# Optimization experiments

Hardware: AMD Instinct MI355X
Metric: run time of the kernel (lower is better)

Reference implementation:

```python
import jax, jax.numpy as jnp
from jax import lax
import numpy as np

N_QUBITS = 4
N_LAYERS = 2


def _apply_gate(state, M, w):
    # state: [B, 2,2,2,2]; M: [2,2] shared or [B,2,2] batched; acts on wire w
    s = jnp.moveaxis(state, w + 1, 1)
    if M.ndim == 3:
        s = jnp.einsum('bij,bj...->bi...', M, s)
    else:
        s = jnp.einsum('ij,bj...->bi...', M, s)
    return jnp.moveaxis(s, 1, w + 1)


def _apply_cnot(state, c, t):
    # c < t always (chain CNOTs). Move control axis to 1; target axis (t+1) unchanged.
    s = jnp.moveaxis(state, c + 1, 1)
    s0 = s[:, 0]
    s1 = jnp.flip(s[:, 1], axis=t)  # target axis after dropping axis1 is t+1-1 = t
    s = jnp.stack([s0, s1], axis=1)
    return jnp.moveaxis(s, 1, c + 1)


def _quantum_head(q_input, qparams):
    # q_input: [B, n_qubits] rotation angles; qparams: [n_layers, n_qubits, 3]
    B = q_input.shape[0]
    state = jnp.zeros((B, 2 ** N_QUBITS), jnp.complex64).at[:, 0].set(1.0)
    state = state.reshape((B,) + (2,) * N_QUBITS)
    # RY feature map (batched matrices)
    for i in range(N_QUBITS):
        th = q_input[:, i]
        c, s = jnp.cos(th / 2), jnp.sin(th / 2)
        M = jnp.stack([jnp.stack([c, -s], -1), jnp.stack([s, c], -1)], -2)  # [B,2,2]
        state = _apply_gate(state, M.astype(jnp.complex64), i)
    # variational layers
    for layer in range(N_LAYERS):
        for i in range(N_QUBITS):
            phi = qparams[layer, i, 0]
            th = qparams[layer, i, 1]
            om = qparams[layer, i, 2]
            c, s = jnp.cos(th / 2), jnp.sin(th / 2)
            hs, hd = 0.5 * (phi + om), 0.5 * (phi - om)
            M = jnp.stack([
                jnp.stack([jnp.exp(-1j * hs) * c, -jnp.exp(1j * hd) * s]),
                jnp.stack([jnp.exp(-1j * hd) * s, jnp.exp(1j * hs) * c]),
            ])  # [2,2] shared across batch (Rot = RZ(om) RY(th) RZ(phi))
            state = _apply_gate(state, M.astype(jnp.complex64), i)
        for i in range(N_QUBITS - 1):
            state = _apply_cnot(state, i, i + 1)
    # <Z_0> = P(q0=0) - P(q0=1)
    probs = state.real ** 2 + state.imag ** 2
    probs = probs.reshape(B, 2, -1)
    return probs[:, 0].sum(-1) - probs[:, 1].sum(-1)


def _maxpool21(x):
    return lax.reduce_window(x, -np.inf, lax.max, (1, 1, 2, 2), (1, 1, 1, 1), 'VALID')


def setup_inputs() -> dict:
    key = jax.random.key(0)
    ks = jax.random.split(key, 8)
    r = lambda k, s, sc: jax.random.normal(k, s, jnp.float32) * sc
    return {
        'inputs': jax.random.normal(ks[0], (128, 3, 250, 250), jnp.float32),
        'conv1_w': r(ks[1], (6, 3, 5, 5), 0.1),
        'conv1_b': jnp.zeros((6,), jnp.float32),
        'conv2_w': r(ks[2], (15, 6, 3, 3), 0.1),
        'conv2_b': jnp.zeros((15,), jnp.float32),
        'fc1_w': r(ks[3], (120, 55815), 0.004),
        'fc1_b': jnp.zeros((120,), jnp.float32),
        'fc2_w': r(ks[4], (84, 120), 0.09),
        'fc2_b': jnp.zeros((84,), jnp.float32),
        'fc3_w': r(ks[5], (1, 84), 0.1),
        'fc3_b': jnp.zeros((1,), jnp.float32),
        'qparams': jax.random.normal(ks[6], (N_LAYERS, N_QUBITS, 3), jnp.float32),
    }


def reference(inputs, conv1_w, conv1_b, conv2_w, conv2_b, fc1_w, fc1_b,
              fc2_w, fc2_b, fc3_w, fc3_b, qparams):
    dn = ('NCHW', 'OIHW', 'NCHW')
    x = lax.conv_general_dilated(inputs, conv1_w, (2, 2), [(1, 1), (1, 1)],
                                 dimension_numbers=dn) + conv1_b[None, :, None, None]
    x = _maxpool21(jax.nn.relu(x))          # [B,6,123,123]
    x = lax.conv_general_dilated(x, conv2_w, (2, 2), [(1, 1), (1, 1)],
                                 dimension_numbers=dn) + conv2_b[None, :, None, None]
    x = _maxpool21(jax.nn.relu(x))          # [B,15,61,61]
    x = x.reshape(x.shape[0], -1)           # [B,55815]
    x = jax.nn.relu(x @ fc1_w.T + fc1_b)
    x = jax.nn.relu(x @ fc2_w.T + fc2_b)
    x = (x @ fc3_w.T + fc3_b)[:, 0]         # [B]
    q_input = jnp.repeat(x[:, None], N_QUBITS, axis=1)
    q_out = _quantum_head(q_input, qparams)  # [B]
    probs = 0.5 * (q_out + 1.0)
    return jnp.stack([probs, 1.0 - probs], axis=-1)
```

## Files before the change

kernel.cpp:

```cpp
#include <hip/hip_runtime.h>

#define SPLITK 256
#define FC1_K 55815
#define KP 55816

__device__ __forceinline__ unsigned short f2bf(float f) {
    unsigned u = __float_as_uint(f);
    return (unsigned short)((u + 0x7FFFu + ((u >> 16) & 1u)) >> 16);
}

__global__ __launch_bounds__(256) void conv1f_k(const float* __restrict__ in,
                                                const float* __restrict__ w,
                                                const float* __restrict__ bias,
                                                float* __restrict__ out) {
    __shared__ float sbuf[4608];
    const int tc = blockIdx.x, tr = blockIdx.y, b = blockIdx.z;
    const int pr0 = tr * 31, pc0 = tc * 31;
    const int tid = threadIdx.x;
    const int i = tid >> 4, j = tid & 15;
    const float* inb = in + (size_t)b * 187500;
    const int ir0 = 2 * pr0 - 1, ic0 = 2 * pc0 - 1;

    float acc[6][2][2];
    #pragma unroll
    for (int o = 0; o < 6; ++o) {
        float bv = bias[o];
        acc[o][0][0] = bv; acc[o][0][1] = bv; acc[o][1][0] = bv; acc[o][1][1] = bv;
    }

    float stg[18];
    auto load_ch = [&](int c) {
        const float* cp = inb + c * 62500;
        int y = tid / 68;
        int x = tid - y * 68;
        #pragma unroll
        for (int it = 0; it < 18; ++it) {
            int gr = ir0 + y, gc = ic0 + x;
            float v = 0.0f;
            if ((unsigned)gr < 250u && (unsigned)gc < 250u)
                v = cp[gr * 250 + gc];
            stg[it] = v;
            x += 52; y += 3;
            if (x >= 68) { x -= 68; ++y; }
        }
    };
    auto write_ch = [&]() {
        #pragma unroll
        for (int it = 0; it < 18; ++it) sbuf[tid + it * 256] = stg[it];
    };
    auto compute_ch = [&](int c) {
        #pragma unroll
        for (int wr = 0; wr < 7; ++wr) {
            const float* rp = &sbuf[(4 * i + wr) * 68 + 4 * j];
            float row[7];
            float4 v4 = *(const float4*)rp;
            float2 v2 = *(const float2*)(rp + 4);
            row[0] = v4.x; row[1] = v4.y; row[2] = v4.z; row[3] = v4.w;
            row[4] = v2.x; row[5] = v2.y; row[6] = rp[6];
            #pragma unroll
            for (int o = 0; o < 6; ++o) {
                #pragma unroll
                for (int kw = 0; kw < 5; ++kw) {
                    if (wr <= 4) {
                        float wv = w[o * 75 + c * 25 + wr * 5 + kw];
                        acc[o][0][0] = fmaf(row[kw], wv, acc[o][0][0]);
                        acc[o][0][1] = fmaf(row[kw + 2], wv, acc[o][0][1]);
                    }
                    if (wr >= 2) {
                        float wv = w[o * 75 + c * 25 + (wr - 2) * 5 + kw];
                        acc[o][1][0] = fmaf(row[kw], wv, acc[o][1][0]);
                        acc[o][1][1] = fmaf(row[kw + 2], wv, acc[o][1][1]);
                    }
                }
            }
        }
    };

    load_ch(0); write_ch();
    __syncthreads();
    load_ch(1); compute_ch(0);
    __syncthreads();
    write_ch();
    __syncthreads();
    load_ch(2); compute_ch(1);
    __syncthreads();
    write_ch();
    __syncthreads();
    compute_ch(2);
    __syncthreads();

    const int gr0 = pr0 + 2 * i, gc0 = pc0 + 2 * j;
    const bool r1in = (2 * i + 1 < 31) && (gr0 + 1 < 123);
    const bool c1in = (2 * j + 1 < 31) && (gc0 + 1 < 123);
    const bool r0in = gr0 < 123, c0in = gc0 < 123;
    #pragma unroll
    for (int g = 0; g < 2; ++g) {
        #pragma unroll
        for (int oo = 0; oo < 3; ++oo)
            #pragma unroll
            for (int di = 0; di < 2; ++di)
                #pragma unroll
                for (int dj = 0; dj < 2; ++dj)
                    sbuf[(oo * 32 + 2 * i + di) * 33 + (2 * j + dj)] =
                        fmaxf(acc[g * 3 + oo][di][dj], 0.0f);
        __syncthreads();
        #pragma unroll
        for (int oo = 0; oo < 3; ++oo) {
            int o = g * 3 + oo;
            const float* p0 = &sbuf[(oo * 32 + 2 * i) * 33 + 2 * j];
            float c00 = p0[0],  c01 = p0[1],  c02 = p0[2];
            float c10 = p0[33], c11 = p0[34], c12 = p0[35];
            float c20 = p0[66], c21 = p0[67], c22 = p0[68];
            float* orow = out + ((size_t)(b * 6 + o) * 123 + gr0) * 123 + gc0;
            if (r0in && c0in) orow[0]   = fmaxf(fmaxf(c00, c01), fmaxf(c10, c11));
            if (r0in && c1in) orow[1]   = fmaxf(fmaxf(c01, c02), fmaxf(c11, c12));
            if (r1in && c0in) orow[123] = fmaxf(fmaxf(c10, c11), fmaxf(c20, c21));
            if (r1in && c1in) orow[124] = fmaxf(fmaxf(c11, c12), fmaxf(c21, c22));
        }
        __syncthreads();
    }
}

__global__ __launch_bounds__(256) void conv2f_k(const float* __restrict__ in,
                                                const float* __restrict__ w,
                                                const float* __restrict__ bias,
                                                unsigned short* __restrict__ out) {
    __shared__ float smem[2000];
    const int tc = blockIdx.x, tr = blockIdx.y, b = blockIdx.z;
    const int pr0 = tr * 15, pc0 = tc * 15;
    const int tid = threadIdx.x;
    const int wv = tid >> 6, lane = tid & 63;
    const int ti = tid >> 4, tj = tid & 15;
    const int tl = ti & 3;
    float* wreg = smem + wv * 320;
    float* halo = smem + 1280;
    const float* inb = in + (size_t)b * 6 * 15129;
    const int irw = 2 * pr0 - 1 + 8 * wv;
    const int ic0 = 2 * pc0 - 1;
    const bool safe = (tr >= 1 && tr <= 3) && (tc >= 1 && tc <= 3);

    int off[5];
    unsigned msk = 0u;
    {
        int y = (lane >= 34) ? 1 : 0;
        int x = lane - 34 * y;
        #pragma unroll
        for (int it = 0; it < 5; ++it) {
            int gr = irw + y, gc = ic0 + x;
            bool valid = ((unsigned)gr < 123u) && ((unsigned)gc < 123u);
            off[it] = valid ? (gr * 123 + gc) : 0;
            msk |= (valid ? 1u : 0u) << it;
            x += 30; ++y;
            if (x >= 34) { x -= 34; ++y; }
        }
    }

    float acc[15];
    #pragma unroll
    for (int o = 0; o < 15; ++o) acc[o] = bias[o];

    for (int c = 0; c < 6; ++c) {
        const float* cp = inb + c * 15129;
        if (safe) {
            #pragma unroll
            for (int it = 0; it < 5; ++it) wreg[lane + it * 64] = cp[off[it]];
        } else {
            #pragma unroll
            for (int it = 0; it < 5; ++it) {
                float v = 0.0f;
                if ((msk >> it) & 1u) v = cp[off[it]];
                wreg[lane + it * 64] = v;
            }
        }
        #pragma unroll
        for (int kh = 0; kh < 3; ++kh) {
            const float* r = &wreg[(2 * tl + kh) * 34 + 2 * tj];
            float a0 = r[0], a1 = r[1], a2 = r[2];
            #pragma unroll
            for (int o = 0; o < 15; ++o) {
                const float* wr_ = &w[o * 54 + c * 9 + kh * 3];
                acc[o] = fmaf(a0, wr_[0], acc[o]);
                acc[o] = fmaf(a1, wr_[1], acc[o]);
                acc[o] = fmaf(a2, wr_[2], acc[o]);
            }
        }
    }

    if (tl == 0 && wv > 0) {
        #pragma unroll
        for (int o = 0; o < 15; ++o)
            halo[(wv - 1) * 240 + o * 16 + tj] = acc[o];
    }
    __syncthreads();

    const int gr = pr0 + ti, gc = pc0 + tj;
    const bool valid = (ti < 15) && (tj < 15) && (gr < 61) && (gc < 61);
    const bool lastrow = (tl == 3);
    const int hb = (wv < 2 ? wv : 2) * 240;
    #pragma unroll
    for (int o = 0; o < 15; ++o) {
        float c00 = acc[o];
        float c01 = __shfl(acc[o], lane + 1);
        float s10 = __shfl(acc[o], lane + 16);
        float s11 = __shfl(acc[o], lane + 17);
        float h10 = halo[hb + o * 16 + tj];
        float h11 = halo[hb + o * 16 + (tj + 1 > 15 ? 15 : tj + 1)];
        float c10 = lastrow ? h10 : s10;
        float c11 = lastrow ? h11 : s11;
        float m = fmaxf(fmaxf(fmaxf(c00, c01), fmaxf(c10, c11)), 0.0f);
        if (valid) out[(size_t)b * KP + o * 3721 + gr * 61 + gc] = f2bf(m);
    }
}

__global__ __launch_bounds__(256) void wcvt_k(const float* __restrict__ W,
                                              unsigned short* __restrict__ Wb) {
    const int n = blockIdx.y;
    const float* src = W + (size_t)n * FC1_K;
    unsigned int* dst = (unsigned int*)(Wb + (size_t)n * KP);
    int base = blockIdx.x * 2048 + threadIdx.x * 2;
    #pragma unroll
    for (int p = 0; p < 4; ++p) {
        int k2 = base + p * 512;
        if (k2 < FC1_K) {
            float v0 = src[k2];
            float v1 = (k2 + 1 < FC1_K) ? src[k2 + 1] : 0.0f;
            dst[k2 >> 1] = (unsigned)f2bf(v0) | ((unsigned)f2bf(v1) << 16);
        }
    }
}

__global__ __launch_bounds__(256) void fc1_k(const unsigned short* __restrict__ Xb,
                                             const unsigned short* __restrict__ Wb,
                                             float* __restrict__ P) {
    using short8 = __attribute__((ext_vector_type(8))) short;
    using f32x4 = __attribute__((ext_vector_type(4))) float;
    __shared__ unsigned short Xs[2][128][40];
    __shared__ unsigned short Ws[2][128][40];
    const int s = blockIdx.x;
    const int ks = s * 224;
    const int ke = min(ks + 224, FC1_K);
    const int tid = threadIdx.x;
    const int row = tid >> 1, cb = (tid & 1) * 16;
    const int wv = tid >> 6, lane = tid & 63;
    const int kb = lane >> 4, lr = lane & 15;

    f32x4 acc[2][8];
    #pragma unroll
    for (int mt = 0; mt < 2; ++mt)
        #pragma unroll
        for (int nt = 0; nt < 8; ++nt)
            acc[mt][nt] = (f32x4){0.f, 0.f, 0.f, 0.f};

    const int nsteps = (ke > ks) ? ((ke - ks + 31) >> 5) : 0;

    auto stage = [&](int buf, int st) {
        const int k0 = ks + st * 32;
        const int krem = ke - k0;
        const unsigned short* xsrc = Xb + (size_t)row * KP + k0 + cb;
        #pragma unroll
        for (int q = 0; q < 2; ++q) {
            int g = cb + q * 8;
            if (g + 8 <= krem) {
                *(uint4*)&Xs[buf][row][g] = *(const uint4*)(xsrc + q * 8);
            } else {
                #pragma unroll
                for (int jj = 0; jj < 8; ++jj)
                    Xs[buf][row][g + jj] = (g + jj < krem) ? xsrc[q * 8 + jj] : (unsigned short)0;
            }
        }
        if (row < 120) {
            const unsigned short* wsrc = Wb + (size_t)row * KP + k0 + cb;
            #pragma unroll
            for (int q = 0; q < 2; ++q) {
                int g = cb + q * 8;
                if (g + 8 <= krem) {
                    *(uint4*)&Ws[buf][row][g] = *(const uint4*)(wsrc + q * 8);
                } else {
                    #pragma unroll
                    for (int jj = 0; jj < 8; ++jj)
                        Ws[buf][row][g + jj] = (g + jj < krem) ? wsrc[q * 8 + jj] : (unsigned short)0;
                }
            }
        } else {
            uint4 z = {0u, 0u, 0u, 0u};
            *(uint4*)&Ws[buf][row][cb] = z;
            *(uint4*)&Ws[buf][row][cb + 8] = z;
        }
    };

    if (nsteps > 0) stage(0, 0);
    int cur = 0;
    for (int st = 0; st < nsteps; ++st) {
        __syncthreads();
        if (st + 1 < nsteps) stage(cur ^ 1, st + 1);
        short8 afr[2];
        #pragma unroll
        for (int mt = 0; mt < 2; ++mt)
            afr[mt] = *(const short8*)&Xs[cur][(wv * 2 + mt) * 16 + lr][kb * 8];
        #pragma unroll
        for (int nt = 0; nt < 8; ++nt) {
            short8 bfr = *(const short8*)&Ws[cur][nt * 16 + lr][kb * 8];
            #pragma unroll
            for (int mt = 0; mt < 2; ++mt)
                acc[mt][nt] = __builtin_amdgcn_mfma_f32_16x16x32_bf16(afr[mt], bfr, acc[mt][nt], 0, 0, 0);
        }
        cur ^= 1;
    }

    float* Pp = P + (size_t)s * 15360;
    #pragma unroll
    for (int mt = 0; mt < 2; ++mt)
        #pragma unroll
        for (int nt = 0; nt < 8; ++nt)
            #pragma unroll
            for (int r = 0; r < 4; ++r) {
                int m = (wv * 2 + mt) * 16 + kb * 4 + r;
                int n = nt * 16 + lr;
                if (n < 120) Pp[m * 120 + n] = acc[mt][nt][r];
            }
}

__global__ __launch_bounds__(512) void tail_k(const float* __restrict__ P,
                                              const float* __restrict__ f1b,
                                              const float* __restrict__ f2w,
                                              const float* __restrict__ f2b,
                                              const float* __restrict__ f3w,
                                              const float* __restrict__ f3b,
                                              const float* __restrict__ qp,
                                              float* __restrict__ out) {
    __shared__ float red[4][120];
    __shared__ float x1[120];
    __shared__ float x2[84];
    int b = blockIdx.x, tid = threadIdx.x;
    if (tid < 480) {
        int part = tid / 120;
        int n = tid - part * 120;
        const float* p = P + (size_t)b * 120 + n;
        float acc = 0.0f;
        #pragma unroll 8
        for (int s = part; s < SPLITK; s += 4)
            acc += p[(size_t)s * 15360];
        red[part][n] = acc;
    }
    __syncthreads();
    if (tid < 120)
        x1[tid] = fmaxf((red[0][tid] + red[1][tid]) + (red[2][tid] + red[3][tid]) + f1b[tid], 0.0f);
    __syncthreads();
    if (tid < 84) {
        float acc = f2b[tid];
        const float* wr = f2w + tid * 120;
        #pragma unroll 4
        for (int n = 0; n < 120; ++n) acc = fmaf(x1[n], wr[n], acc);
        x2[tid] = fmaxf(acc, 0.0f);
    }
    __syncthreads();
    if (tid == 0) {
        float x = f3b[0];
        for (int m = 0; m < 84; ++m) x = fmaf(x2[m], f3w[m], x);
        float sr[16], si[16];
        #pragma unroll
        for (int i = 0; i < 16; ++i) { sr[i] = 0.0f; si[i] = 0.0f; }
        sr[0] = 1.0f;
        float c0 = cosf(0.5f * x), s0 = sinf(0.5f * x);
        #pragma unroll
        for (int w = 0; w < 4; ++w) {
            int mask = 8 >> w;
            #pragma unroll
            for (int idx = 0; idx < 16; ++idx) {
                if (idx & mask) continue;
                int i1 = idx | mask;
                float a0r = sr[idx], a0i = si[idx], a1r = sr[i1], a1i = si[i1];
                sr[idx] = c0 * a0r - s0 * a1r;  si[idx] = c0 * a0i - s0 * a1i;
                sr[i1]  = s0 * a0r + c0 * a1r;  si[i1]  = s0 * a0i + c0 * a1i;
            }
        }
        for (int layer = 0; layer < 2; ++layer) {
            #pragma unroll
            for (int w = 0; w < 4; ++w) {
                int gi = (layer * 4 + w) * 3;
                float phi = qp[gi], th = qp[gi + 1], om = qp[gi + 2];
                float hs = 0.5f * (phi + om), hd = 0.5f * (phi - om);
                float ct = cosf(0.5f * th), st = sinf(0.5f * th);
                float chs = cosf(hs), shs = sinf(hs);
                float chd = cosf(hd), shd = sinf(hd);
                float m00r = chs * ct,  m00i = -shs * ct;
                float m01r = -chd * st, m01i = -shd * st;
                float m10r = chd * st,  m10i = -shd * st;
                float m11r = chs * ct,  m11i = shs * ct;
                int mask = 8 >> w;
                #pragma unroll
                for (int idx = 0; idx < 16; ++idx) {
                    if (idx & mask) continue;
                    int i1 = idx | mask;
                    float a0r = sr[idx], a0i = si[idx], a1r = sr[i1], a1i = si[i1];
                    sr[idx] = m00r * a0r - m00i * a0i + m01r * a1r - m01i * a1i;
                    si[idx] = m00r * a0i + m00i * a0r + m01r * a1i + m01i * a1r;
                    sr[i1]  = m10r * a0r - m10i * a0i + m11r * a1r - m11i * a1i;
                    si[i1]  = m10r * a0i + m10i * a0r + m11r * a1i + m11i * a1r;
                }
            }
            #pragma unroll
            for (int cw = 0; cw < 3; ++cw) {
                int cm = 8 >> cw, tm = 8 >> (cw + 1);
                #pragma unroll
                for (int idx = 0; idx < 16; ++idx) {
                    if ((idx & cm) && !(idx & tm)) {
                        int i1 = idx | tm;
                        float tr = sr[idx]; sr[idx] = sr[i1]; sr[i1] = tr;
                        float ti = si[idx]; si[idx] = si[i1]; si[i1] = ti;
                    }
                }
            }
        }
        float q = 0.0f;
        #pragma unroll
        for (int idx = 0; idx < 16; ++idx) {
            float p2 = sr[idx] * sr[idx] + si[idx] * si[idx];
            q += (idx < 8) ? p2 : -p2;
        }
        float pr = 0.5f * (q + 1.0f);
        out[2 * b] = pr;
        out[2 * b + 1] = 1.0f - pr;
    }
}

extern "C" void kernel_launch(void* const* d_in, const int* in_sizes, int n_in,
                              void* d_out, int out_size, void* d_ws, size_t ws_size,
                              hipStream_t stream) {
    const float* inp = (const float*)d_in[0];
    const float* c1w = (const float*)d_in[1];
    const float* c1b = (const float*)d_in[2];
    const float* c2w = (const float*)d_in[3];
    const float* c2b = (const float*)d_in[4];
    const float* f1w = (const float*)d_in[5];
    const float* f1b = (const float*)d_in[6];
    const float* f2w = (const float*)d_in[7];
    const float* f2b = (const float*)d_in[8];
    const float* f3w = (const float*)d_in[9];
    const float* f3b = (const float*)d_in[10];
    const float* qp  = (const float*)d_in[11];
    float* out = (float*)d_out;
    float* ws = (float*)d_ws;

    float* B = ws;
    unsigned short* Db = (unsigned short*)(ws + 11619072);
    float* P = ws + 15191296;
    unsigned short* Wb = (unsigned short*)(ws + 19123456);

    wcvt_k<<<dim3(28, 120), 256, 0, stream>>>(f1w, Wb);
    conv1f_k<<<dim3(4, 4, 128), 256, 0, stream>>>(inp, c1w, c1b, B);
    conv2f_k<<<dim3(5, 5, 128), 256, 0, stream>>>(B, c2w, c2b, Db);
    fc1_k<<<dim3(SPLITK), 256, 0, stream>>>(Db, Wb, P);
    tail_k<<<128, 512, 0, stream>>>(P, f1b, f2w, f2b, f3w, f3b, qp, out);
}
```

Baseline: 144.0 us.

## Fuse fc1 weight bf16 conversion into GEMM staging; process two images per conv2 block

Drops the separate weight-conversion kernel. fc1 now reads the fp32 weights directly and packs them to bf16 while staging into shared memory, which removes one launch and the round trip of the bf16 weight copy through memory. In exchange, fc1 reads twice the weight bytes and uses scalar, bounds-checked loads instead of 16-byte vector loads. conv2 blocks now loop over two images each with half the grid, and add an extra barrier per image.

```diff
diff --git a/kernel.cpp b/kernel.cpp
--- a/kernel.cpp
+++ b/kernel.cpp
@@ -126,7 +126,7 @@
                                                 const float* __restrict__ bias,
                                                 unsigned short* __restrict__ out) {
     __shared__ float smem[2000];
-    const int tc = blockIdx.x, tr = blockIdx.y, b = blockIdx.z;
+    const int tc = blockIdx.x, tr = blockIdx.y, b0 = blockIdx.z;
     const int pr0 = tr * 15, pc0 = tc * 15;
     const int tid = threadIdx.x;
     const int wv = tid >> 6, lane = tid & 63;
@@ -134,7 +134,6 @@
     const int tl = ti & 3;
     float* wreg = smem + wv * 320;
     float* halo = smem + 1280;
-    const float* inb = in + (size_t)b * 6 * 15129;
     const int irw = 2 * pr0 - 1 + 8 * wv;
     const int ic0 = 2 * pc0 - 1;
     const bool safe = (tr >= 1 && tr <= 3) && (tc >= 1 && tc <= 3);
@@ -155,82 +154,71 @@
         }
     }
 
-    float acc[15];
-    #pragma unroll
-    for (int o = 0; o < 15; ++o) acc[o] = bias[o];
-
-    for (int c = 0; c < 6; ++c) {
-        const float* cp = inb + c * 15129;
-        if (safe) {
-            #pragma unroll
-            for (int it = 0; it < 5; ++it) wreg[lane + it * 64] = cp[off[it]];
-        } else {
-            #pragma unroll
-            for (int it = 0; it < 5; ++it) {
-                float v = 0.0f;
-                if ((msk >> it) & 1u) v = cp[off[it]];
-                wreg[lane + it * 64] = v;
-            }
-        }
-        #pragma unroll
-        for (int kh = 0; kh < 3; ++kh) {
-            const float* r = &wreg[(2 * tl + kh) * 34 + 2 * tj];
-            float a0 = r[0], a1 = r[1], a2 = r[2];
-            #pragma unroll
-            for (int o = 0; o < 15; ++o) {
-                const float* wr_ = &w[o * 54 + c * 9 + kh * 3];
-                acc[o] = fmaf(a0, wr_[0], acc[o]);
-                acc[o] = fmaf(a1, wr_[1], acc[o]);
-                acc[o] = fmaf(a2, wr_[2], acc[o]);
-            }
-        }
-    }
-
-    if (tl == 0 && wv > 0) {
-        #pragma unroll
-        for (int o = 0; o < 15; ++o)
-            halo[(wv - 1) * 240 + o * 16 + tj] = acc[o];
-    }
-    __syncthreads();
-
-    const int gr = pr0 + ti, gc = pc0 + tj;
-    const bool valid = (ti < 15) && (tj < 15) && (gr < 61) && (gc < 61);
-    const bool lastrow = (tl == 3);
-    const int hb = (wv < 2 ? wv : 2) * 240;
-    #pragma unroll
-    for (int o = 0; o < 15; ++o) {
-        float c00 = acc[o];
-        float c01 = __shfl(acc[o], lane + 1);
-        float s10 = __shfl(acc[o], lane + 16);
-        float s11 = __shfl(acc[o], lane + 17);
-        float h10 = halo[hb + o * 16 + tj];
-        float h11 = halo[hb + o * 16 + (tj + 1 > 15 ? 15 : tj + 1)];
-        float c10 = lastrow ? h10 : s10;
-        float c11 = lastrow ? h11 : s11;
-        float m = fmaxf(fmaxf(fmaxf(c00, c01), fmaxf(c10, c11)), 0.0f);
-        if (valid) out[(size_t)b * KP + o * 3721 + gr * 61 + gc] = f2bf(m);
-    }
-}
-
-__global__ __launch_bounds__(256) void wcvt_k(const float* __restrict__ W,
-                                              unsigned short* __restrict__ Wb) {
-    const int n = blockIdx.y;
-    const float* src = W + (size_t)n * FC1_K;
-    unsigned int* dst = (unsigned int*)(Wb + (size_t)n * KP);
-    int base = blockIdx.x * 2048 + threadIdx.x * 2;
-    #pragma unroll
-    for (int p = 0; p < 4; ++p) {
-        int k2 = base + p * 512;
-        if (k2 < FC1_K) {
-            float v0 = src[k2];
-            float v1 = (k2 + 1 < FC1_K) ? src[k2 + 1] : 0.0f;
-            dst[k2 >> 1] = (unsigned)f2bf(v0) | ((unsigned)f2bf(v1) << 16);
-        }
+    for (int ip = 0; ip < 2; ++ip) {
+        const int b = b0 + 64 * ip;
+        const float* inb = in + (size_t)b * 6 * 15129;
+
+        float acc[15];
+        #pragma unroll
+        for (int o = 0; o < 15; ++o) acc[o] = bias[o];
+
+        for (int c = 0; c < 6; ++c) {
+            const float* cp = inb + c * 15129;
+            if (safe) {
+                #pragma unroll
+                for (int it = 0; it < 5; ++it) wreg[lane + it * 64] = cp[off[it]];
+            } else {
+                #pragma unroll
+                for (int it = 0; it < 5; ++it) {
+                    float v = 0.0f;
+                    if ((msk >> it) & 1u) v = cp[off[it]];
+                    wreg[lane + it * 64] = v;
+                }
+            }
+            #pragma unroll
+            for (int kh = 0; kh < 3; ++kh) {
+                const float* r = &wreg[(2 * tl + kh) * 34 + 2 * tj];
+                float a0 = r[0], a1 = r[1], a2 = r[2];
+                #pragma unroll
+                for (int o = 0; o < 15; ++o) {
+                    const float* wr_ = &w[o * 54 + c * 9 + kh * 3];
+                    acc[o] = fmaf(a0, wr_[0], acc[o]);
+                    acc[o] = fmaf(a1, wr_[1], acc[o]);
+                    acc[o] = fmaf(a2, wr_[2], acc[o]);
+                }
+            }
+        }
+
+        if (tl == 0 && wv > 0) {
+            #pragma unroll
+            for (int o = 0; o < 15; ++o)
+                halo[(wv - 1) * 240 + o * 16 + tj] = acc[o];
+        }
+        __syncthreads();
+
+        const int gr = pr0 + ti, gc = pc0 + tj;
+        const bool valid = (ti < 15) && (tj < 15) && (gr < 61) && (gc < 61);
+        const bool lastrow = (tl == 3);
+        const int hb = (wv < 2 ? wv : 2) * 240;
+        #pragma unroll
+        for (int o = 0; o < 15; ++o) {
+            float c00 = acc[o];
+            float c01 = __shfl(acc[o], lane + 1);
+            float s10 = __shfl(acc[o], lane + 16);
+            float s11 = __shfl(acc[o], lane + 17);
+            float h10 = halo[hb + o * 16 + tj];
+            float h11 = halo[hb + o * 16 + (tj + 1 > 15 ? 15 : tj + 1)];
+            float c10 = lastrow ? h10 : s10;
+            float c11 = lastrow ? h11 : s11;
+            float m = fmaxf(fmaxf(fmaxf(c00, c01), fmaxf(c10, c11)), 0.0f);
+            if (valid) out[(size_t)b * KP + o * 3721 + gr * 61 + gc] = f2bf(m);
+        }
+        __syncthreads();
     }
 }
 
 __global__ __launch_bounds__(256) void fc1_k(const unsigned short* __restrict__ Xb,
-                                             const unsigned short* __restrict__ Wb,
+                                             const float* __restrict__ Wf,
                                              float* __restrict__ P) {
     using short8 = __attribute__((ext_vector_type(8))) short;
     using f32x4 = __attribute__((ext_vector_type(4))) float;
@@ -269,17 +257,19 @@
             }
         }
         if (row < 120) {
-            const unsigned short* wsrc = Wb + (size_t)row * KP + k0 + cb;
+            const float* wsrc = Wf + (size_t)row * FC1_K + k0 + cb;
             #pragma unroll
             for (int q = 0; q < 2; ++q) {
                 int g = cb + q * 8;
-                if (g + 8 <= krem) {
-                    *(uint4*)&Ws[buf][row][g] = *(const uint4*)(wsrc + q * 8);
-                } else {
-                    #pragma unroll
-                    for (int jj = 0; jj < 8; ++jj)
-                        Ws[buf][row][g + jj] = (g + jj < krem) ? wsrc[q * 8 + jj] : (unsigned short)0;
-                }
+                unsigned pk[4];
+                #pragma unroll
+                for (int h = 0; h < 4; ++h) {
+                    float v0 = (g + 2 * h     < krem) ? wsrc[q * 8 + 2 * h]     : 0.0f;
+                    float v1 = (g + 2 * h + 1 < krem) ? wsrc[q * 8 + 2 * h + 1] : 0.0f;
+                    pk[h] = (unsigned)f2bf(v0) | ((unsigned)f2bf(v1) << 16);
+                }
+                uint4 u = {pk[0], pk[1], pk[2], pk[3]};
+                *(uint4*)&Ws[buf][row][g] = u;
             }
         } else {
             uint4 z = {0u, 0u, 0u, 0u};
@@ -445,11 +435,9 @@
     float* B = ws;
     unsigned short* Db = (unsigned short*)(ws + 11619072);
     float* P = ws + 15191296;
-    unsigned short* Wb = (unsigned short*)(ws + 19123456);
-
-    wcvt_k<<<dim3(28, 120), 256, 0, stream>>>(f1w, Wb);
+
     conv1f_k<<<dim3(4, 4, 128), 256, 0, stream>>>(inp, c1w, c1b, B);
-    conv2f_k<<<dim3(5, 5, 128), 256, 0, stream>>>(B, c2w, c2b, Db);
-    fc1_k<<<dim3(SPLITK), 256, 0, stream>>>(Db, Wb, P);
+    conv2f_k<<<dim3(5, 5, 64), 256, 0, stream>>>(B, c2w, c2b, Db);
+    fc1_k<<<dim3(SPLITK), 256, 0, stream>>>(Db, f1w, P);
     tail_k<<<128, 512, 0, stream>>>(P, f1b, f2w, f2b, f3w, f3b, qp, out);
 }
```

Result: no change. 146.8 us (+2.0%).
